# Performance work log

Measured on AMD Instinct MI355X. Metric: run time of the kernel, lower is better.

Reference implementation:

```python
import jax, jax.numpy as jnp
import numpy as np

D_MODEL = 1024
H = 16
D_K = D_MODEL // H


def setup_inputs() -> dict:
    key = jax.random.key(0)
    ks = jax.random.split(key, 8)
    B, S = 2, 2048
    scale = 1.0 / np.sqrt(D_MODEL)
    return {
        "query": jax.random.normal(ks[0], (B, S, D_MODEL), dtype=jnp.float32),
        "key": jax.random.normal(ks[1], (B, S, D_MODEL), dtype=jnp.float32),
        "value": jax.random.normal(ks[2], (B, S, D_MODEL), dtype=jnp.float32),
        "mask": jnp.ones((B, 1, 1, S), dtype=jnp.int32),
        "Wq": jax.random.normal(ks[3], (D_MODEL, D_MODEL), dtype=jnp.float32) * scale,
        "Wk": jax.random.normal(ks[4], (D_MODEL, D_MODEL), dtype=jnp.float32) * scale,
        "Wv": jax.random.normal(ks[5], (D_MODEL, D_MODEL), dtype=jnp.float32) * scale,
        "Wo": jax.random.normal(ks[6], (D_MODEL, D_MODEL), dtype=jnp.float32) * scale,
    }


def reference(query, key, value, mask, Wq, Wk, Wv, Wo):
    # mask is a no-op in the original (masked_fill result discarded); dropout=0.
    B, S, _ = query.shape
    q = (query @ Wq.T).reshape(B, S, H, D_K)  # [B,S,H,Dk]
    k = (key @ Wk.T).reshape(B, S, H, D_K)
    v = (value @ Wv.T).reshape(B, S, H, D_K)
    # scores = Q K^T / sqrt(d_k)  -- NOTE: no softmax in the source module
    scores = jnp.einsum("bqhd,bkhd->bhqk", q, k) / jnp.sqrt(jnp.float32(D_K))
    out = jnp.einsum("bhqk,bkhd->bqhd", scores, v).reshape(B, S, D_MODEL)
    return out @ Wo.T
```

## Files before the change

kernel.cpp:

```cpp
#include <hip/hip_runtime.h>

#define DEV __device__ __forceinline__

typedef __attribute__((ext_vector_type(8))) short short8;
typedef __attribute__((ext_vector_type(4))) float f32x4;

DEV short f2bf(float x) {
  unsigned u = __float_as_uint(x);
  unsigned r = (u + 0x7fffu + ((u >> 16) & 1u)) >> 16;
  return (short)r;
}
DEV float bf2f(short x) {
  return __uint_as_float(((unsigned)(unsigned short)x) << 16);
}

DEV void gload_lds16(const void* g, void* l) {
  __builtin_amdgcn_global_load_lds((const __attribute__((address_space(1))) void*)g,
                                   (__attribute__((address_space(3))) void*)l, 16, 0, 0);
}

__global__ __launch_bounds__(256) void cvt_bf16(const float* __restrict__ in,
                                                short* __restrict__ out, int n8) {
  int i = blockIdx.x * 256 + threadIdx.x;
  if (i >= n8) return;
  const float4* p = reinterpret_cast<const float4*>(in) + (size_t)i * 2;
  float4 a = p[0], b = p[1];
  short8 o;
  o[0] = f2bf(a.x); o[1] = f2bf(a.y); o[2] = f2bf(a.z); o[3] = f2bf(a.w);
  o[4] = f2bf(b.x); o[5] = f2bf(b.y); o[6] = f2bf(b.z); o[7] = f2bf(b.w);
  *reinterpret_cast<short8*>(out + (size_t)i * 8) = o;
}

template <typename OutT>
__global__ __launch_bounds__(256) void gemm_bt(const short* __restrict__ A,
                                               const short* __restrict__ W,
                                               OutT* __restrict__ C, int M) {
  __shared__ short At[128 * 64];
  __shared__ short Bt[64 * 64];
  const int t = threadIdx.x;
  const int w = t >> 6;
  const int l = t & 63;
  const int lg = l >> 4, lr = l & 15;
  const int wm = w >> 1, wn = w & 1;
  const int rowBase = blockIdx.y * 128;
  const int colBase = blockIdx.x * 64;
  (void)M;

  f32x4 acc[4][2] = {};

  for (int kt = 0; kt < 16; ++kt) {
    const int k0 = kt * 64;
    __syncthreads();
#pragma unroll
    for (int i = 0; i < 4; ++i) {
      int c = w * 256 + i * 64 + l;
      int r = c >> 3, s = c & 7;
      const short* src = A + (size_t)(rowBase + r) * 1024 + k0 + ((s ^ (r & 7)) << 3);
      gload_lds16(src, At + (size_t)(w * 256 + i * 64) * 8);
    }
#pragma unroll
    for (int i = 0; i < 2; ++i) {
      int c = w * 128 + i * 64 + l;
      int r = c >> 3, s = c & 7;
      const short* src = W + (size_t)(colBase + r) * 1024 + k0 + ((s ^ (r & 7)) << 3);
      gload_lds16(src, Bt + (size_t)(w * 128 + i * 64) * 8);
    }
    __syncthreads();
#pragma unroll
    for (int kk = 0; kk < 2; ++kk) {
      short8 bfr[2];
#pragma unroll
      for (int n = 0; n < 2; ++n) {
        int br = wn * 32 + n * 16 + lr;
        int slot = (kk * 4 + lg) ^ (br & 7);
        bfr[n] = *reinterpret_cast<const short8*>(&Bt[br * 64 + slot * 8]);
      }
#pragma unroll
      for (int m = 0; m < 4; ++m) {
        int ar = wm * 64 + m * 16 + lr;
        int slot = (kk * 4 + lg) ^ (ar & 7);
        short8 afr = *reinterpret_cast<const short8*>(&At[ar * 64 + slot * 8]);
        acc[m][0] = __builtin_amdgcn_mfma_f32_16x16x32_bf16(afr, bfr[0], acc[m][0], 0, 0, 0);
        acc[m][1] = __builtin_amdgcn_mfma_f32_16x16x32_bf16(afr, bfr[1], acc[m][1], 0, 0, 0);
      }
    }
  }
#pragma unroll
  for (int m = 0; m < 4; ++m)
#pragma unroll
    for (int n = 0; n < 2; ++n) {
      int row0 = rowBase + wm * 64 + m * 16 + lg * 4;
      int col = colBase + wn * 32 + n * 16 + lr;
#pragma unroll
      for (int j = 0; j < 4; ++j) {
        float v = acc[m][n][j];
        if constexpr (sizeof(OutT) == 2)
          C[(size_t)(row0 + j) * 1024 + col] = (OutT)f2bf(v);
        else
          C[(size_t)(row0 + j) * 1024 + col] = (OutT)v;
      }
    }
}

__global__ __launch_bounds__(256) void kv_outer(const short* __restrict__ Kp,
                                                const short* __restrict__ Vp,
                                                float* __restrict__ Mb) {
  __shared__ float Ks[128][64];
  __shared__ float Vs[128][64];
  const int t = threadIdx.x;
  const int sc = blockIdx.x, h = blockIdx.y, b = blockIdx.z;
  const size_t base = ((size_t)(b * 2048 + sc * 128)) * 1024 + h * 64;
  for (int e = t; e < 128 * 64; e += 256) {
    int r = e >> 6, c = e & 63;
    size_t g = base + (size_t)r * 1024 + c;
    Ks[r][c] = bf2f(Kp[g]);
    Vs[r][c] = bf2f(Vp[g]);
  }
  __syncthreads();
  const int dp0 = (t >> 4) * 4, d0 = (t & 15) * 4;
  float acc[4][4] = {};
  for (int s = 0; s < 128; ++s) {
    float4 kv = *reinterpret_cast<const float4*>(&Ks[s][dp0]);
    float4 vv = *reinterpret_cast<const float4*>(&Vs[s][d0]);
    float ka[4] = {kv.x, kv.y, kv.z, kv.w};
    float va[4] = {vv.x, vv.y, vv.z, vv.w};
#pragma unroll
    for (int i = 0; i < 4; ++i)
#pragma unroll
      for (int j = 0; j < 4; ++j) acc[i][j] += ka[i] * va[j];
  }
  float* dst = Mb + (size_t)(b * 16 + h) * 4096;
#pragma unroll
  for (int i = 0; i < 4; ++i)
#pragma unroll
    for (int j = 0; j < 4; ++j)
      atomicAdd(&dst[(dp0 + i) * 64 + d0 + j], acc[i][j] * 0.125f);
}

__global__ __launch_bounds__(256) void make_w2t(const float* __restrict__ Mb,
                                                const short* __restrict__ Wo,
                                                short* __restrict__ W2T) {
  __shared__ float Ms[64][65];
  __shared__ float Wos[64][64];
  const int t = threadIdx.x;
  const int jc = blockIdx.x, h = blockIdx.y, b = blockIdx.z;
  const float* Msrc = Mb + (size_t)(b * 16 + h) * 4096;
  for (int e = t; e < 4096; e += 256) {
    int r = e >> 6, c = e & 63;
    Ms[r][c] = Msrc[e];
    Wos[r][c] = bf2f(Wo[(size_t)(jc * 64 + r) * 1024 + h * 64 + c]);
  }
  __syncthreads();
  const int j0 = (t >> 4) * 4, p0 = (t & 15) * 4;
  float acc[4][4] = {};
  for (int d = 0; d < 64; ++d) {
    float wv[4], mv[4];
#pragma unroll
    for (int i = 0; i < 4; ++i) { wv[i] = Wos[j0 + i][d]; mv[i] = Ms[p0 + i][d]; }
#pragma unroll
    for (int i = 0; i < 4; ++i)
#pragma unroll
      for (int j2 = 0; j2 < 4; ++j2) acc[i][j2] += wv[i] * mv[j2];
  }
  short* dst = W2T + (size_t)b * 1048576;
#pragma unroll
  for (int i = 0; i < 4; ++i)
#pragma unroll
    for (int j2 = 0; j2 < 4; ++j2)
      dst[(size_t)(jc * 64 + j0 + i) * 1024 + h * 64 + p0 + j2] = f2bf(acc[i][j2]);
}

extern "C" void kernel_launch(void* const* d_in, const int* in_sizes, int n_in,
                              void* d_out, int out_size, void* d_ws, size_t ws_size,
                              hipStream_t stream) {
  const float* q  = (const float*)d_in[0];
  const float* k  = (const float*)d_in[1];
  const float* v  = (const float*)d_in[2];
  const float* Wq = (const float*)d_in[4];
  const float* Wk = (const float*)d_in[5];
  const float* Wv = (const float*)d_in[6];
  const float* Wo = (const float*)d_in[7];
  float* out = (float*)d_out;
  char* ws = (char*)d_ws;

  short* xbf = (short*)(ws);
  short* wqb = (short*)(ws + (8l << 20));
  short* wkb = wqb + 1048576;
  short* wvb = wkb + 1048576;
  short* wob = wvb + 1048576;
  short* Qp  = (short*)(ws + (16l << 20));
  short* Kp  = (short*)(ws + (24l << 20));
  short* Vp  = (short*)(ws + (32l << 20));
  float* Mb  = (float*)(ws + (40l << 20));
  short* W2T = (short*)(ws + (40l << 20) + (1l << 19));

  hipMemsetAsync(Mb, 0, 32 * 64 * 64 * sizeof(float), stream);

  cvt_bf16<<<512, 256, 0, stream>>>(Wq, wqb, 131072);
  cvt_bf16<<<512, 256, 0, stream>>>(Wk, wkb, 131072);
  cvt_bf16<<<512, 256, 0, stream>>>(Wv, wvb, 131072);
  cvt_bf16<<<512, 256, 0, stream>>>(Wo, wob, 131072);

  cvt_bf16<<<2048, 256, 0, stream>>>(q, xbf, 524288);
  gemm_bt<short><<<dim3(16, 32), 256, 0, stream>>>(xbf, wqb, Qp, 4096);
  cvt_bf16<<<2048, 256, 0, stream>>>(k, xbf, 524288);
  gemm_bt<short><<<dim3(16, 32), 256, 0, stream>>>(xbf, wkb, Kp, 4096);
  cvt_bf16<<<2048, 256, 0, stream>>>(v, xbf, 524288);
  gemm_bt<short><<<dim3(16, 32), 256, 0, stream>>>(xbf, wvb, Vp, 4096);

  kv_outer<<<dim3(16, 16, 2), 256, 0, stream>>>(Kp, Vp, Mb);
  make_w2t<<<dim3(16, 16, 2), 256, 0, stream>>>(Mb, wob, W2T);

  gemm_bt<float><<<dim3(16, 16), 256, 0, stream>>>(Qp, W2T, out, 2048);
  gemm_bt<float><<<dim3(16, 16), 256, 0, stream>>>(Qp + (size_t)2048 * 1024, W2T + 1048576,
                                                   out + (size_t)2048 * 1024, 2048);
}
```

Measured before the change: 259.9 us.

## Batch conversions and projections into single launches with 128x128 GEMM tiles

The seven fp32-to-bf16 conversion launches are merged into one kernel that picks its source and destination by global index. The three Q/K/V projection GEMMs become one launch using blockIdx.z with strides, and the two output GEMMs become another. The GEMM tile grows from 128x64 to 128x128, with a 4x4 MFMA accumulator per wave. The aim is to cut launch count and serialization, raise data reuse per tile, and fill the GPU better. The cost is more registers and LDS per block, plus fewer blocks for the output GEMM.

```diff
diff --git a/kernel.cpp b/kernel.cpp
--- a/kernel.cpp
+++ b/kernel.cpp
@@ -19,34 +19,55 @@
                                    (__attribute__((address_space(3))) void*)l, 16, 0, 0);
 }
 
-__global__ __launch_bounds__(256) void cvt_bf16(const float* __restrict__ in,
-                                                short* __restrict__ out, int n8) {
-  int i = blockIdx.x * 256 + threadIdx.x;
-  if (i >= n8) return;
-  const float4* p = reinterpret_cast<const float4*>(in) + (size_t)i * 2;
+__global__ __launch_bounds__(256) void cvt_all(
+    const float* __restrict__ s0, const float* __restrict__ s1,
+    const float* __restrict__ s2, const float* __restrict__ s3,
+    const float* __restrict__ s4, const float* __restrict__ s5,
+    const float* __restrict__ s6,
+    short* __restrict__ d0, short* __restrict__ d1, short* __restrict__ d2,
+    short* __restrict__ d3, short* __restrict__ d4, short* __restrict__ d5,
+    short* __restrict__ d6) {
+  int g = blockIdx.x * 256 + threadIdx.x;
+  const float* s;
+  short* d;
+  int off;
+  if (g < 524288) { s = s0; d = d0; off = g; }
+  else if (g < 1048576) { s = s1; d = d1; off = g - 524288; }
+  else if (g < 1572864) { s = s2; d = d2; off = g - 1048576; }
+  else {
+    int w2 = g - 1572864;
+    int seg = w2 >> 17;
+    off = w2 & 131071;
+    s = seg == 0 ? s3 : seg == 1 ? s4 : seg == 2 ? s5 : s6;
+    d = seg == 0 ? d3 : seg == 1 ? d4 : seg == 2 ? d5 : d6;
+  }
+  const float4* p = reinterpret_cast<const float4*>(s) + (size_t)off * 2;
   float4 a = p[0], b = p[1];
   short8 o;
   o[0] = f2bf(a.x); o[1] = f2bf(a.y); o[2] = f2bf(a.z); o[3] = f2bf(a.w);
   o[4] = f2bf(b.x); o[5] = f2bf(b.y); o[6] = f2bf(b.z); o[7] = f2bf(b.w);
-  *reinterpret_cast<short8*>(out + (size_t)i * 8) = o;
+  *reinterpret_cast<short8*>(d + (size_t)off * 8) = o;
 }
 
 template <typename OutT>
-__global__ __launch_bounds__(256) void gemm_bt(const short* __restrict__ A,
-                                               const short* __restrict__ W,
-                                               OutT* __restrict__ C, int M) {
+__global__ __launch_bounds__(256) void gemm_bt128(const short* __restrict__ A,
+                                                  const short* __restrict__ W,
+                                                  OutT* __restrict__ C,
+                                                  long strideA, long strideW, long strideC) {
   __shared__ short At[128 * 64];
-  __shared__ short Bt[64 * 64];
+  __shared__ short Bt[128 * 64];
+  const short* Ab = A + (size_t)blockIdx.z * strideA;
+  const short* Wb = W + (size_t)blockIdx.z * strideW;
+  OutT* Cb = C + (size_t)blockIdx.z * strideC;
   const int t = threadIdx.x;
   const int w = t >> 6;
   const int l = t & 63;
   const int lg = l >> 4, lr = l & 15;
   const int wm = w >> 1, wn = w & 1;
   const int rowBase = blockIdx.y * 128;
-  const int colBase = blockIdx.x * 64;
-  (void)M;
-
-  f32x4 acc[4][2] = {};
+  const int colBase = blockIdx.x * 128;
+
+  f32x4 acc[4][4] = {};
 
   for (int kt = 0; kt < 16; ++kt) {
     const int k0 = kt * 64;
@@ -55,49 +76,46 @@
     for (int i = 0; i < 4; ++i) {
       int c = w * 256 + i * 64 + l;
       int r = c >> 3, s = c & 7;
-      const short* src = A + (size_t)(rowBase + r) * 1024 + k0 + ((s ^ (r & 7)) << 3);
-      gload_lds16(src, At + (size_t)(w * 256 + i * 64) * 8);
-    }
-#pragma unroll
-    for (int i = 0; i < 2; ++i) {
-      int c = w * 128 + i * 64 + l;
-      int r = c >> 3, s = c & 7;
-      const short* src = W + (size_t)(colBase + r) * 1024 + k0 + ((s ^ (r & 7)) << 3);
-      gload_lds16(src, Bt + (size_t)(w * 128 + i * 64) * 8);
+      int goff = k0 + ((s ^ (r & 7)) << 3);
+      gload_lds16(Ab + (size_t)(rowBase + r) * 1024 + goff, At + (size_t)c * 8);
+      gload_lds16(Wb + (size_t)(colBase + r) * 1024 + goff, Bt + (size_t)c * 8);
     }
     __syncthreads();
 #pragma unroll
     for (int kk = 0; kk < 2; ++kk) {
-      short8 bfr[2];
-#pragma unroll
-      for (int n = 0; n < 2; ++n) {
-        int br = wn * 32 + n * 16 + lr;
+      short8 afr[4], bfr[4];
+#pragma unroll
+      for (int m = 0; m < 4; ++m) {
+        int ar = wm * 64 + m * 16 + lr;
+        int slot = (kk * 4 + lg) ^ (ar & 7);
+        afr[m] = *reinterpret_cast<const short8*>(&At[ar * 64 + slot * 8]);
+      }
+#pragma unroll
+      for (int n = 0; n < 4; ++n) {
+        int br = wn * 64 + n * 16 + lr;
         int slot = (kk * 4 + lg) ^ (br & 7);
         bfr[n] = *reinterpret_cast<const short8*>(&Bt[br * 64 + slot * 8]);
       }
 #pragma unroll
-      for (int m = 0; m < 4; ++m) {
-        int ar = wm * 64 + m * 16 + lr;
-        int slot = (kk * 4 + lg) ^ (ar & 7);
-        short8 afr = *reinterpret_cast<const short8*>(&At[ar * 64 + slot * 8]);
-        acc[m][0] = __builtin_amdgcn_mfma_f32_16x16x32_bf16(afr, bfr[0], acc[m][0], 0, 0, 0);
-        acc[m][1] = __builtin_amdgcn_mfma_f32_16x16x32_bf16(afr, bfr[1], acc[m][1], 0, 0, 0);
-      }
+      for (int m = 0; m < 4; ++m)
+#pragma unroll
+        for (int n = 0; n < 4; ++n)
+          acc[m][n] = __builtin_amdgcn_mfma_f32_16x16x32_bf16(afr[m], bfr[n], acc[m][n], 0, 0, 0);
     }
   }
 #pragma unroll
   for (int m = 0; m < 4; ++m)
 #pragma unroll
-    for (int n = 0; n < 2; ++n) {
+    for (int n = 0; n < 4; ++n) {
       int row0 = rowBase + wm * 64 + m * 16 + lg * 4;
-      int col = colBase + wn * 32 + n * 16 + lr;
+      int col = colBase + wn * 64 + n * 16 + lr;
 #pragma unroll
       for (int j = 0; j < 4; ++j) {
         float v = acc[m][n][j];
         if constexpr (sizeof(OutT) == 2)
-          C[(size_t)(row0 + j) * 1024 + col] = (OutT)f2bf(v);
+          Cb[(size_t)(row0 + j) * 1024 + col] = (OutT)f2bf(v);
         else
-          C[(size_t)(row0 + j) * 1024 + col] = (OutT)v;
+          Cb[(size_t)(row0 + j) * 1024 + col] = (OutT)v;
       }
     }
 }
@@ -183,35 +201,33 @@
   float* out = (float*)d_out;
   char* ws = (char*)d_ws;
 
-  short* xbf = (short*)(ws);
-  short* wqb = (short*)(ws + (8l << 20));
-  short* wkb = wqb + 1048576;
-  short* wvb = wkb + 1048576;
-  short* wob = wvb + 1048576;
-  short* Qp  = (short*)(ws + (16l << 20));
-  short* Kp  = (short*)(ws + (24l << 20));
-  short* Vp  = (short*)(ws + (32l << 20));
-  float* Mb  = (float*)(ws + (40l << 20));
-  short* W2T = (short*)(ws + (40l << 20) + (1l << 19));
+  short* qkv = (short*)(ws);
+  short* qb = qkv;
+  short* kb = qkv + (size_t)4194304;
+  short* vb = qkv + (size_t)8388608;
+  short* wb = (short*)(ws + (24l << 20));
+  short* wqb = wb;
+  short* wkb = wb + 1048576;
+  short* wvb = wb + 2097152;
+  short* wob = wb + 3145728;
+  short* Pp = (short*)(ws + (32l << 20));
+  short* Qp = Pp;
+  short* Kp = Pp + (size_t)4194304;
+  short* Vp = Pp + (size_t)8388608;
+  float* Mb  = (float*)(ws + (56l << 20));
+  short* W2T = (short*)(ws + (57l << 20));
 
   hipMemsetAsync(Mb, 0, 32 * 64 * 64 * sizeof(float), stream);
 
-  cvt_bf16<<<512, 256, 0, stream>>>(Wq, wqb, 131072);
-  cvt_bf16<<<512, 256, 0, stream>>>(Wk, wkb, 131072);
-  cvt_bf16<<<512, 256, 0, stream>>>(Wv, wvb, 131072);
-  cvt_bf16<<<512, 256, 0, stream>>>(Wo, wob, 131072);
-
-  cvt_bf16<<<2048, 256, 0, stream>>>(q, xbf, 524288);
-  gemm_bt<short><<<dim3(16, 32), 256, 0, stream>>>(xbf, wqb, Qp, 4096);
-  cvt_bf16<<<2048, 256, 0, stream>>>(k, xbf, 524288);
-  gemm_bt<short><<<dim3(16, 32), 256, 0, stream>>>(xbf, wkb, Kp, 4096);
-  cvt_bf16<<<2048, 256, 0, stream>>>(v, xbf, 524288);
-  gemm_bt<short><<<dim3(16, 32), 256, 0, stream>>>(xbf, wvb, Vp, 4096);
+  cvt_all<<<8192, 256, 0, stream>>>(q, k, v, Wq, Wk, Wv, Wo,
+                                    qb, kb, vb, wqb, wkb, wvb, wob);
+
+  gemm_bt128<short><<<dim3(8, 32, 3), 256, 0, stream>>>(
+      qkv, wb, Pp, 4194304l, 1048576l, 4194304l);
 
   kv_outer<<<dim3(16, 16, 2), 256, 0, stream>>>(Kp, Vp, Mb);
   make_w2t<<<dim3(16, 16, 2), 256, 0, stream>>>(Mb, wob, W2T);
 
-  gemm_bt<float><<<dim3(16, 16), 256, 0, stream>>>(Qp, W2T, out, 2048);
-  gemm_bt<float><<<dim3(16, 16), 256, 0, stream>>>(Qp + (size_t)2048 * 1024, W2T + 1048576,
-                                                   out + (size_t)2048 * 1024, 2048);
-}
+  gemm_bt128<float><<<dim3(8, 16, 2), 256, 0, stream>>>(
+      Qp, W2T, out, 2097152l, 1048576l, 2097152l);
+}
```

Result: faster. 217.7 us (-16.3%).
